# Kernel optimization log

Measured on AMD Instinct MI355X. Metric: run time of the kernel, lower is better.

## Reference

```python
import jax, jax.numpy as jnp
import numpy as np

B, N, M, D = 4, 4096, 4096, 128


def setup_inputs() -> dict:
    key = jax.random.key(0)
    kk, kq, kv = jax.random.split(key, 3)
    return {
        "k": jax.random.normal(kk, (B, N, D), dtype=jnp.float32),
        "q": jax.random.normal(kq, (B, M, D), dtype=jnp.float32),
        "v": jax.random.normal(kv, (B, M, D), dtype=jnp.float32),
    }


def reference(k, q, v):
    # scores: [B, N, M] = k @ q^T
    scores = jnp.einsum("bnd,bmd->bnm", k, q)
    # Original uses nn.Softmax() with no dim; torch's legacy rule resolves
    # dim=0 for 3-D inputs, so softmax is over the batch axis, applied twice.
    w = jax.nn.softmax(jax.nn.softmax(scores, axis=0), axis=0)
    out = jnp.einsum("bnm,bmd->bnd", w, v)
    return out
```

## Files before the change

kernel.cpp:

```cpp
#include <hip/hip_runtime.h>
#include <hip/hip_bf16.h>

#define NB 4
#define NN 4096
#define MM 4096
#define DD 128
#define BN 32
#define BM 64
#define NCH 8
#define OUT_ELEMS ((size_t)NB * NN * DD)

using f32x4  = __attribute__((ext_vector_type(4))) float;
using bf16x8 = __attribute__((ext_vector_type(8))) short;

__device__ __forceinline__ float fast_exp2(float x) {
  return __builtin_amdgcn_exp2f(x);
}

__device__ __forceinline__ int rfl(int x) {
  return __builtin_amdgcn_readfirstlane(x);
}

__device__ __forceinline__ short f2bf(float x) {
  union { __hip_bfloat16 h; short s; } u;
  u.h = __float2bfloat16(x);
  return u.s;
}

__device__ __forceinline__ float bf2f(unsigned short s) {
  union { float f; unsigned u; } u;
  u.u = ((unsigned)s) << 16;
  return u.f;
}

__device__ __forceinline__ bf16x8 pack8(const float* __restrict__ p) {
  float4 a = *(const float4*)p;
  float4 b = *(const float4*)(p + 4);
  bf16x8 r;
  r[0] = f2bf(a.x); r[1] = f2bf(a.y); r[2] = f2bf(a.z); r[3] = f2bf(a.w);
  r[4] = f2bf(b.x); r[5] = f2bf(b.y); r[6] = f2bf(b.z); r[7] = f2bf(b.w);
  return r;
}

__global__ __launch_bounds__(256) void zero_out_kernel(float4* __restrict__ out) {
  out[(size_t)blockIdx.x * 256 + threadIdx.x] = (float4){0.f, 0.f, 0.f, 0.f};
}

__global__ __launch_bounds__(256) void prep_kernel(
    const float* __restrict__ k, const float* __restrict__ q, const float* __restrict__ v,
    unsigned short* __restrict__ kbt, unsigned short* __restrict__ qbt,
    unsigned short* __restrict__ vtt) {
  __shared__ unsigned short t[64][72];
  if (blockIdx.y < 2) {
    const float* src = blockIdx.y ? q : k;
    unsigned short* dst = blockIdx.y ? qbt : kbt;
    const int blk = blockIdx.x;
    const int b = blk >> 8, rf = blk & 255;
    const int kf = threadIdx.x >> 6, l = threadIdx.x & 63;
    const int lr = l & 15, hg = l >> 4;
    const float* s = src + ((size_t)(b * 4096 + rf * 16 + lr) * DD + kf * 32 + hg * 8);
    *(bf16x8*)(dst + (((size_t)((b * 256 + rf) * 4 + kf)) << 9) + (l << 3)) = pack8(s);
    return;
  }
  if (blockIdx.x >= 512) return;
  const int b = blockIdx.x >> 7;
  const int rem = blockIdx.x & 127;
  const int d0 = (rem >> 6) * 64, m0 = (rem & 63) * 64;
  const int r = threadIdx.x >> 2, c4 = threadIdx.x & 3;
  const float* src = v + ((size_t)b * MM + m0 + r) * DD + d0 + c4 * 16;
  for (int j = 0; j < 4; ++j) {
    float4 x = *(const float4*)(src + j * 4);
    int dl = c4 * 16 + j * 4;
    t[dl + 0][r] = (unsigned short)f2bf(x.x);
    t[dl + 1][r] = (unsigned short)f2bf(x.y);
    t[dl + 2][r] = (unsigned short)f2bf(x.z);
    t[dl + 3][r] = (unsigned short)f2bf(x.w);
  }
  __syncthreads();
  const int s8 = threadIdx.x >> 5;
  const int dfl = s8 & 3, mtl = s8 >> 2;
  const int t32 = threadIdx.x & 31;
  for (int ll = 0; ll < 2; ++ll) {
    const int l = t32 * 2 + ll;
    const int lr = l & 15, hg = l >> 4;
    bf16x8 val = *(bf16x8*)&t[dfl * 16 + lr][mtl * 32 + hg * 8];
    *(bf16x8*)(vtt + (((size_t)((b * 8 + (d0 >> 4) + dfl) * 128 + (m0 >> 5) + mtl)) << 9) +
               (l << 3)) = val;
  }
}

__global__ __launch_bounds__(256) void reduce8_frag_kernel(const unsigned short* __restrict__ p,
                                                           float* __restrict__ out) {
  const size_t idx = (size_t)blockIdx.x * 256 + threadIdx.x;
  float r0 = 0.f, r1 = 0.f, r2 = 0.f, r3 = 0.f;
  for (int c = 0; c < NCH; ++c) {
    ushort4 a = *(const ushort4*)(p + (size_t)c * OUT_ELEMS + idx * 4);
    r0 += bf2f(a.x); r1 += bf2f(a.y); r2 += bf2f(a.z); r3 += bf2f(a.w);
  }
  const int l = (int)(idx & 63);
  const int djg = (int)((idx >> 6) & 7);
  const int nf = (int)((idx >> 9) & 255);
  const int bq = (int)(idx >> 17);
  const int lr = l & 15, hg = l >> 4;
  float* o = out + ((size_t)(bq * 4096 + nf * 16 + hg * 4) * DD + djg * 16 + lr);
  o[0] = r0; o[DD] = r1; o[2 * DD] = r2; o[3 * DD] = r3;
}

#define LGKM0_SBAR()                                        \
  do {                                                      \
    asm volatile("s_waitcnt lgkmcnt(0)" ::: "memory");      \
    __builtin_amdgcn_sched_barrier(0);                      \
    __builtin_amdgcn_s_barrier();                           \
  } while (0)

template <bool WS, bool PART>
__global__ __launch_bounds__(512, 4) void attn_fused(
    const float* __restrict__ k, const float* __restrict__ q, const float* __restrict__ v,
    const unsigned short* __restrict__ kbt, const unsigned short* __restrict__ qbt,
    const unsigned short* __restrict__ vtt, void* __restrict__ outp) {
  __shared__ alignas(8)  unsigned short s_pos[NB][8][64][4];
  __shared__ alignas(16) unsigned short Wl[NB][BN][BM];

  const int tid = threadIdx.x;
  const int wv = tid >> 6, l = tid & 63, lr = l & 15, hg = l >> 4;
  const int voff = l << 3;
  const int wg = blockIdx.x;
  const int cid = wg & (NCH - 1);
  const int nt = wg >> 3;
  const int n0 = nt * BN;
  const int it0 = cid * (MM / BM / NCH);
  const int it1 = it0 + (MM / BM / NCH);

  const int bq = wv >> 1, h = wv & 1;
  const int h_s = wv >> 2, fi_s = (wv >> 1) & 1, fj_s = wv & 1;

  bf16x8 ka[2][4];
  {
    const unsigned short* kp = WS ? (kbt + rfl(((bq * 256 + nt * 2) * 4) << 9)) : nullptr;
    for (int fn = 0; fn < 2; ++fn)
      for (int kf = 0; kf < 4; ++kf) {
        if (WS) ka[fn][kf] = *(const bf16x8*)(kp + fn * 2048 + kf * 512 + voff);
        else    ka[fn][kf] = pack8(k + ((size_t)bq * NN + n0 + fn * 16 + lr) * DD +
                                   kf * 32 + hg * 8);
      }
  }

  f32x4 acc[2][4];
  for (int fi = 0; fi < 2; ++fi)
    for (int dj = 0; dj < 4; ++dj) acc[fi][dj] = (f32x4){0.f, 0.f, 0.f, 0.f};

  bf16x8 vf[4][2];
  bf16x8 qf[2][4];

  auto load_q = [&](int it) {
    if (WS) {
      const unsigned short* qp = qbt + rfl(((bq * 256 + it * 4 + h * 2) * 4) << 9);
      for (int fm = 0; fm < 2; ++fm)
        for (int kf = 0; kf < 4; ++kf)
          qf[fm][kf] = *(const bf16x8*)(qp + fm * 2048 + kf * 512 + voff);
    } else {
      const int m0 = it * BM;
      for (int fm = 0; fm < 2; ++fm)
        for (int kf = 0; kf < 4; ++kf)
          qf[fm][kf] = pack8(q + ((size_t)bq * MM + m0 + h * 32 + fm * 16 + lr) * DD +
                             kf * 32 + hg * 8);
    }
  };

  auto qk_mfma = [&]() {
    f32x4 s[2][2];
    for (int fm = 0; fm < 2; ++fm)
      for (int fn = 0; fn < 2; ++fn) s[fm][fn] = (f32x4){0.f, 0.f, 0.f, 0.f};
    __builtin_amdgcn_s_setprio(1);
    for (int kf = 0; kf < 4; ++kf)
      for (int fm = 0; fm < 2; ++fm)
        for (int fn = 0; fn < 2; ++fn)
          s[fm][fn] = __builtin_amdgcn_mfma_f32_16x16x32_bf16(qf[fm][kf], ka[fn][kf],
                                                              s[fm][fn], 0, 0, 0);
    __builtin_amdgcn_s_setprio(0);
    for (int fm = 0; fm < 2; ++fm)
      for (int fn = 0; fn < 2; ++fn) {
        short4 pk;
        pk.x = f2bf(s[fm][fn][0]); pk.y = f2bf(s[fm][fn][1]);
        pk.z = f2bf(s[fm][fn][2]); pk.w = f2bf(s[fm][fn][3]);
        *(short4*)&s_pos[bq][h * 4 + fm * 2 + fn][l][0] = pk;
      }
  };

  auto issue_v = [&](int it) {
    if (WS) {
      const unsigned short* vp = vtt + rfl((((bq * 8 + h * 4) * 128) + it * 2) << 9);
      for (int dj = 0; dj < 4; ++dj)
        for (int kf = 0; kf < 2; ++kf)
          vf[dj][kf] = *(const bf16x8*)(vp + dj * 65536 + kf * 512 + voff);
    } else {
      const int m0 = it * BM;
      for (int dj = 0; dj < 4; ++dj)
        for (int kf = 0; kf < 2; ++kf) {
          bf16x8 t;
          for (int e = 0; e < 8; ++e)
            t[e] = f2bf(v[((size_t)bq * MM + m0 + kf * 32 + hg * 8 + e) * DD +
                          h * 64 + dj * 16 + lr]);
          vf[dj][kf] = t;
        }
    }
  };

  auto do_sm = [&]() {
    float sv[NB][4], w[NB][4];
    for (int bb = 0; bb < NB; ++bb) {
      short4 sp = *(short4*)&s_pos[bb][wv][l][0];
      sv[bb][0] = bf2f((unsigned short)sp.x); sv[bb][1] = bf2f((unsigned short)sp.y);
      sv[bb][2] = bf2f((unsigned short)sp.z); sv[bb][3] = bf2f((unsigned short)sp.w);
    }
    const float L2E = 1.4426950408889634f;
    for (int qq = 0; qq < 4; ++qq) {
      float e0 = fast_exp2(sv[0][qq] * L2E), e1 = fast_exp2(sv[1][qq] * L2E);
      float e2 = fast_exp2(sv[2][qq] * L2E), e3 = fast_exp2(sv[3][qq] * L2E);
      float inv = __builtin_amdgcn_rcpf((e0 + e1) + (e2 + e3)) * L2E;
      float f0 = fast_exp2(e0 * inv), f1 = fast_exp2(e1 * inv);
      float f2v = fast_exp2(e2 * inv), f3 = fast_exp2(e3 * inv);
      float inv2 = __builtin_amdgcn_rcpf((f0 + f1) + (f2v + f3));
      w[0][qq] = f0 * inv2; w[1][qq] = f1 * inv2;
      w[2][qq] = f2v * inv2; w[3][qq] = f3 * inv2;
    }
    const int n_loc = fj_s * 16 + lr;
    const int mchunk = (h_s * 4 + fi_s * 2 + (hg >> 1)) ^ (n_loc & 7);
    const int moff = mchunk * 8 + (hg & 1) * 4;
    for (int bb = 0; bb < NB; ++bb) {
      short4 pk;
      pk.x = f2bf(w[bb][0]); pk.y = f2bf(w[bb][1]);
      pk.z = f2bf(w[bb][2]); pk.w = f2bf(w[bb][3]);
      *(short4*)&Wl[bb][n_loc][moff] = pk;
    }
  };

  auto do_pv = [&]() {
    bf16x8 wf[2][2];
    for (int fi = 0; fi < 2; ++fi)
      for (int kf = 0; kf < 2; ++kf) {
        const int row = fi * 16 + lr, mo = kf * 32 + hg * 8;
        wf[fi][kf] = *(bf16x8*)&Wl[bq][row][mo ^ ((row & 7) << 3)];
      }
    __builtin_amdgcn_s_setprio(1);
    for (int kf = 0; kf < 2; ++kf)
      for (int fi = 0; fi < 2; ++fi)
        for (int dj = 0; dj < 4; ++dj)
          acc[fi][dj] = __builtin_amdgcn_mfma_f32_16x16x32_bf16(wf[fi][kf], vf[dj][kf],
                                                                acc[fi][dj], 0, 0, 0);
    __builtin_amdgcn_s_setprio(0);
  };

  load_q(it0);
  qk_mfma();
  LGKM0_SBAR();
  for (int t = it0; t < it1; ++t) {
    issue_v(t);
    do_sm();
    LGKM0_SBAR();
    do_pv();
    if (t + 1 < it1) {
      load_q(t + 1);
      qk_mfma();
    }
    LGKM0_SBAR();
  }

  if (PART) {
    unsigned short* dst = (unsigned short*)outp + (size_t)cid * OUT_ELEMS +
                          rfl((((bq * 256 + nt * 2) * 8 + h * 4)) << 8);
    for (int fi = 0; fi < 2; ++fi)
      for (int dj = 0; dj < 4; ++dj) {
        short4 pk;
        pk.x = f2bf(acc[fi][dj][0]); pk.y = f2bf(acc[fi][dj][1]);
        pk.z = f2bf(acc[fi][dj][2]); pk.w = f2bf(acc[fi][dj][3]);
        *(short4*)(dst + fi * 2048 + dj * 256 + (l << 2)) = pk;
      }
  } else {
    float* dst = (float*)outp;
    for (int fi = 0; fi < 2; ++fi)
      for (int dj = 0; dj < 4; ++dj)
        for (int qq = 0; qq < 4; ++qq)
          atomicAdd(dst + ((size_t)bq * NN + n0 + fi * 16 + hg * 4 + qq) * DD +
                        h * 64 + dj * 16 + lr,
                    acc[fi][dj][qq]);
  }
}

extern "C" void kernel_launch(void* const* d_in, const int* in_sizes, int n_in,
                              void* d_out, int out_size, void* d_ws, size_t ws_size,
                              hipStream_t stream) {
  (void)in_sizes; (void)n_in; (void)out_size;
  const float* k = (const float*)d_in[0];
  const float* q = (const float*)d_in[1];
  const float* v = (const float*)d_in[2];
  float* out = (float*)d_out;

  const size_t elems = (size_t)NB * MM * DD;
  const size_t need_bf = 3 * elems * sizeof(unsigned short);
  const size_t need_full = need_bf + NCH * OUT_ELEMS * sizeof(unsigned short);
  const bool use_ws = (d_ws != nullptr) && (ws_size >= need_bf);
  const bool use_part = (d_ws != nullptr) && (ws_size >= need_full);

  if (use_ws) {
    unsigned short* kbt = (unsigned short*)d_ws;
    unsigned short* qbt = kbt + elems;
    unsigned short* vtt = qbt + elems;
    prep_kernel<<<dim3(NB * 256, 3), 256, 0, stream>>>(k, q, v, kbt, qbt, vtt);
    if (use_part) {
      unsigned short* partials = vtt + elems;
      attn_fused<true, true><<<dim3(NN / BN * NCH), 512, 0, stream>>>(k, q, v, kbt, qbt, vtt,
                                                                      (void*)partials);
      reduce8_frag_kernel<<<2048, 256, 0, stream>>>(partials, out);
    } else {
      zero_out_kernel<<<(NB * NN * DD) / 4 / 256, 256, 0, stream>>>((float4*)out);
      attn_fused<true, false><<<dim3(NN / BN * NCH), 512, 0, stream>>>(k, q, v, kbt, qbt, vtt,
                                                                       (void*)out);
    }
  } else {
    zero_out_kernel<<<(NB * NN * DD) / 4 / 256, 256, 0, stream>>>((float4*)out);
    attn_fused<false, false><<<dim3(NN / BN * NCH), 512, 0, stream>>>(k, q, v, nullptr,
                                                                      nullptr, nullptr,
                                                                      (void*)out);
  }
}
```

Measured before the change: 76.95 us.

## Double-buffer scores and weights to overlap softmax with PV, halve M-chunks

The main loop becomes software-pipelined with double-buffered LDS for the score tile and the weight tile. Softmax of iteration t now runs alongside the PV MFMA of iteration t-1, and the V fragment loads for t are issued at the end of the iteration, so each iteration needs one barrier instead of two. Separately, the number of M-chunks per N tile drops from 8 to 4, which halves the bf16 partial-output traffic and the reduction work but doubles the loop length per block and halves the grid. LDS use per block doubles, which may lower how many blocks fit on each CU.

```diff
diff --git a/kernel.cpp b/kernel.cpp
--- a/kernel.cpp
+++ b/kernel.cpp
@@ -7,7 +7,7 @@
 #define DD 128
 #define BN 32
 #define BM 64
-#define NCH 8
+#define NCH 4
 #define OUT_ELEMS ((size_t)NB * NN * DD)
 
 using f32x4  = __attribute__((ext_vector_type(4))) float;
@@ -89,7 +89,7 @@
   }
 }
 
-__global__ __launch_bounds__(256) void reduce8_frag_kernel(const unsigned short* __restrict__ p,
+__global__ __launch_bounds__(256) void reduce4_frag_kernel(const unsigned short* __restrict__ p,
                                                            float* __restrict__ out) {
   const size_t idx = (size_t)blockIdx.x * 256 + threadIdx.x;
   float r0 = 0.f, r1 = 0.f, r2 = 0.f, r3 = 0.f;
@@ -118,15 +118,15 @@
     const float* __restrict__ k, const float* __restrict__ q, const float* __restrict__ v,
     const unsigned short* __restrict__ kbt, const unsigned short* __restrict__ qbt,
     const unsigned short* __restrict__ vtt, void* __restrict__ outp) {
-  __shared__ alignas(8)  unsigned short s_pos[NB][8][64][4];
-  __shared__ alignas(16) unsigned short Wl[NB][BN][BM];
+  __shared__ alignas(8)  unsigned short s_pos[2][NB][8][64][4];
+  __shared__ alignas(16) unsigned short Wl[2][NB][BN][BM];
 
   const int tid = threadIdx.x;
   const int wv = tid >> 6, l = tid & 63, lr = l & 15, hg = l >> 4;
   const int voff = l << 3;
   const int wg = blockIdx.x;
   const int cid = wg & (NCH - 1);
-  const int nt = wg >> 3;
+  const int nt = wg >> 2;
   const int n0 = nt * BN;
   const int it0 = cid * (MM / BM / NCH);
   const int it1 = it0 + (MM / BM / NCH);
@@ -167,7 +167,7 @@
     }
   };
 
-  auto qk_mfma = [&]() {
+  auto qk_mfma = [&](int buf) {
     f32x4 s[2][2];
     for (int fm = 0; fm < 2; ++fm)
       for (int fn = 0; fn < 2; ++fn) s[fm][fn] = (f32x4){0.f, 0.f, 0.f, 0.f};
@@ -183,7 +183,7 @@
         short4 pk;
         pk.x = f2bf(s[fm][fn][0]); pk.y = f2bf(s[fm][fn][1]);
         pk.z = f2bf(s[fm][fn][2]); pk.w = f2bf(s[fm][fn][3]);
-        *(short4*)&s_pos[bq][h * 4 + fm * 2 + fn][l][0] = pk;
+        *(short4*)&s_pos[buf][bq][h * 4 + fm * 2 + fn][l][0] = pk;
       }
   };
 
@@ -206,10 +206,10 @@
     }
   };
 
-  auto do_sm = [&]() {
+  auto do_sm = [&](int buf) {
     float sv[NB][4], w[NB][4];
     for (int bb = 0; bb < NB; ++bb) {
-      short4 sp = *(short4*)&s_pos[bb][wv][l][0];
+      short4 sp = *(short4*)&s_pos[buf][bb][wv][l][0];
       sv[bb][0] = bf2f((unsigned short)sp.x); sv[bb][1] = bf2f((unsigned short)sp.y);
       sv[bb][2] = bf2f((unsigned short)sp.z); sv[bb][3] = bf2f((unsigned short)sp.w);
     }
@@ -231,16 +231,16 @@
       short4 pk;
       pk.x = f2bf(w[bb][0]); pk.y = f2bf(w[bb][1]);
       pk.z = f2bf(w[bb][2]); pk.w = f2bf(w[bb][3]);
-      *(short4*)&Wl[bb][n_loc][moff] = pk;
-    }
-  };
-
-  auto do_pv = [&]() {
+      *(short4*)&Wl[buf][bb][n_loc][moff] = pk;
+    }
+  };
+
+  auto do_pv = [&](int buf) {
     bf16x8 wf[2][2];
     for (int fi = 0; fi < 2; ++fi)
       for (int kf = 0; kf < 2; ++kf) {
         const int row = fi * 16 + lr, mo = kf * 32 + hg * 8;
-        wf[fi][kf] = *(bf16x8*)&Wl[bq][row][mo ^ ((row & 7) << 3)];
+        wf[fi][kf] = *(bf16x8*)&Wl[buf][bq][row][mo ^ ((row & 7) << 3)];
       }
     __builtin_amdgcn_s_setprio(1);
     for (int kf = 0; kf < 2; ++kf)
@@ -252,19 +252,20 @@
   };
 
   load_q(it0);
-  qk_mfma();
+  qk_mfma(it0 & 1);
   LGKM0_SBAR();
   for (int t = it0; t < it1; ++t) {
-    issue_v(t);
-    do_sm();
-    LGKM0_SBAR();
-    do_pv();
+    do_sm(t & 1);
+    if (t > it0) do_pv((t - 1) & 1);
     if (t + 1 < it1) {
       load_q(t + 1);
-      qk_mfma();
-    }
+      qk_mfma((t + 1) & 1);
+    }
+    __builtin_amdgcn_sched_barrier(0);
+    issue_v(t);
     LGKM0_SBAR();
   }
+  do_pv((it1 - 1) & 1);
 
   if (PART) {
     unsigned short* dst = (unsigned short*)outp + (size_t)cid * OUT_ELEMS +
@@ -311,7 +312,7 @@
       unsigned short* partials = vtt + elems;
       attn_fused<true, true><<<dim3(NN / BN * NCH), 512, 0, stream>>>(k, q, v, kbt, qbt, vtt,
                                                                       (void*)partials);
-      reduce8_frag_kernel<<<2048, 256, 0, stream>>>(partials, out);
+      reduce4_frag_kernel<<<2048, 256, 0, stream>>>(partials, out);
     } else {
       zero_out_kernel<<<(NB * NN * DD) / 4 / 256, 256, 0, stream>>>((float4*)out);
       attn_fused<true, false><<<dim3(NN / BN * NCH), 512, 0, stream>>>(k, q, v, kbt, qbt, vtt,
```

After: 74.41 us. 1.03x faster.
